# Kernel optimization log

Hardware: AMD Instinct MI355X
Metric: run time of the kernel (lower is better)

The kernel has to match this reference:

```python
import jax, jax.numpy as jnp
import numpy as np

N = 50000   # nodes
E = 800000  # edges (avg degree 16)
D = 128     # in_features == out_features (residual)
NEG_SLOPE = 0.2
BN_EPS = 1e-5


def setup_inputs() -> dict:
    key = jax.random.key(0)
    ks = jax.random.split(key, 8)
    x = jax.random.normal(ks[0], (N, D), jnp.float32)
    edge_index = jax.random.randint(ks[1], (2, E), 0, N, dtype=jnp.int32)
    W = jax.random.normal(ks[2], (D, D), jnp.float32) * 0.05
    att_src = jax.random.normal(ks[3], (D,), jnp.float32) * 0.1
    att_dst = jax.random.normal(ks[4], (D,), jnp.float32) * 0.1
    bias = jax.random.normal(ks[5], (D,), jnp.float32) * 0.01
    gamma = jnp.ones((D,), jnp.float32) + jax.random.normal(ks[6], (D,), jnp.float32) * 0.05
    beta = jax.random.normal(ks[7], (D,), jnp.float32) * 0.05
    return {"x": x, "edge_index": edge_index, "W": W, "att_src": att_src,
            "att_dst": att_dst, "bias": bias, "gamma": gamma, "beta": beta}


def reference(x, edge_index, W, att_src, att_dst, bias, gamma, beta):
    src, dst = edge_index[0], edge_index[1]
    # Linear transform (GATConv lin)
    h = x @ W                                   # [N, D]
    # Per-node attention logit halves
    a_s = h @ att_src                           # [N]
    a_d = h @ att_dst                           # [N]
    # Per-edge logits + LeakyReLU
    e = jax.nn.leaky_relu(a_s[src] + a_d[dst], NEG_SLOPE)  # [E]
    # Segment softmax over destination neighborhoods
    m = jax.ops.segment_max(e, dst, num_segments=N)        # [N]
    m = jnp.where(jnp.isfinite(m), m, 0.0)
    p = jnp.exp(e - m[dst])                                 # [E]
    denom = jax.ops.segment_sum(p, dst, num_segments=N)    # [N]
    alpha = p / denom[dst]                                  # [E]
    # Scatter-aggregate weighted neighbor features
    y = jax.ops.segment_sum(alpha[:, None] * h[src], dst, num_segments=N)  # [N, D]
    y = y + bias
    # NormDropRes (eval mode): BN with running_mean=0, running_var=1; dropout off
    yn = gamma * (y / jnp.sqrt(1.0 + BN_EPS)) + beta
    yn = jax.nn.relu(yn)
    # residual: in==out so base = x
    return x + yn
```

## Files before the change

kernel.cpp:

```cpp
#include <hip/hip_runtime.h>
#include <math.h>

#define NN 50000
#define EE 800000
#define DD 128
#define NEG 0.2f
#define SLOT 48
#define NWIN 512
#define WIN 98
#define CAP 2048

typedef short bf16x8 __attribute__((ext_vector_type(8)));
typedef float f32x4  __attribute__((ext_vector_type(4)));
typedef int   i32x4  __attribute__((ext_vector_type(4)));

__device__ __forceinline__ unsigned short f2bf(float f) {
    unsigned u = __float_as_uint(f);
    unsigned r = u + 0x7fffu + ((u >> 16) & 1u);
    return (unsigned short)(r >> 16);
}

__global__ __launch_bounds__(256) void k_pre(
        const float* __restrict__ W, unsigned short* __restrict__ wt,
        int* __restrict__ win_cnt)
{
    const int t = threadIdx.x;
    if (blockIdx.x == 64) {
        for (int i = t; i < NWIN; i += 256) win_cnt[i] = 0;
        return;
    }
    int idx = blockIdx.x * 256 + t;
    int k = idx >> 7, n = idx & 127;
    wt[n * DD + k] = f2bf(W[idx]);
}

#define XS_STRIDE 136
__global__ __launch_bounds__(256) void k_A(
        const float* __restrict__ x, const unsigned short* __restrict__ wtg,
        const float* __restrict__ att_src, const float* __restrict__ att_dst,
        unsigned short* __restrict__ hb, float* __restrict__ a_s, float* __restrict__ a_d,
        const int* __restrict__ ei, int* __restrict__ win_cnt, unsigned* __restrict__ pairs)
{
    __shared__ __align__(16) short smem[26112];
    const int t = threadIdx.x;

    if (blockIdx.x & 1) {
        int* lcnt  = (int*)smem;
        int* lbase = (int*)smem + NWIN;
        for (int i = t; i < NWIN; i += 256) lcnt[i] = 0;
        __syncthreads();

        int idx = (int)(blockIdx.x >> 1) * 256 + t;
        int b[4], lp[4];
        unsigned v[4];
        bool valid = idx < EE / 4;
        if (valid) {
            i32x4 s4 = __builtin_nontemporal_load(&((const i32x4*)ei)[idx]);
            i32x4 d4 = __builtin_nontemporal_load(&((const i32x4*)(ei + EE))[idx]);
            b[0] = d4.x / WIN; v[0] = ((unsigned)(d4.x - b[0] * WIN) << 16) | (unsigned)s4.x;
            b[1] = d4.y / WIN; v[1] = ((unsigned)(d4.y - b[1] * WIN) << 16) | (unsigned)s4.y;
            b[2] = d4.z / WIN; v[2] = ((unsigned)(d4.z - b[2] * WIN) << 16) | (unsigned)s4.z;
            b[3] = d4.w / WIN; v[3] = ((unsigned)(d4.w - b[3] * WIN) << 16) | (unsigned)s4.w;
            lp[0] = atomicAdd(&lcnt[b[0]], 1);
            lp[1] = atomicAdd(&lcnt[b[1]], 1);
            lp[2] = atomicAdd(&lcnt[b[2]], 1);
            lp[3] = atomicAdd(&lcnt[b[3]], 1);
        }
        __syncthreads();
        for (int i = t; i < NWIN; i += 256) {
            int c = lcnt[i];
            lbase[i] = c ? atomicAdd(&win_cnt[i], c) : 0;
        }
        __syncthreads();
        if (valid) {
#pragma unroll
            for (int k = 0; k < 4; k++) {
                int pos = lbase[b[k]] + lp[k];
                if (pos < CAP) pairs[(size_t)b[k] * CAP + pos] = v[k];
            }
        }
        return;
    }

    short* xs = smem;
    short* ws = smem + 64 * XS_STRIDE;
    const int row0 = (int)(blockIdx.x >> 1) * 64;

#pragma unroll
    for (int i = 0; i < 4; i++) {
        int idx = t + i * 256;
        int m = idx >> 4, c = idx & 15;
        int row = row0 + m;
        float4 f0 = make_float4(0.f, 0.f, 0.f, 0.f), f1 = f0;
        if (row < NN) {
            const float* p = x + (size_t)row * DD + c * 8;
            f0 = *(const float4*)p;
            f1 = *(const float4*)(p + 4);
        }
        bf16x8 v;
        v[0] = (short)f2bf(f0.x); v[1] = (short)f2bf(f0.y);
        v[2] = (short)f2bf(f0.z); v[3] = (short)f2bf(f0.w);
        v[4] = (short)f2bf(f1.x); v[5] = (short)f2bf(f1.y);
        v[6] = (short)f2bf(f1.z); v[7] = (short)f2bf(f1.w);
        *(bf16x8*)&xs[m * XS_STRIDE + c * 8] = v;
    }
#pragma unroll
    for (int i = 0; i < 8; i++) {
        int idx = t + i * 256;
        int n = idx >> 4, c = idx & 15;
        uint4 v = ((const uint4*)wtg)[idx];
        *(uint4*)&ws[n * XS_STRIDE + c * 8] = v;
    }
    __syncthreads();

    const int wv = t >> 6;
    const int lane = t & 63;
    const int n0 = lane & 15;
    const int quad = lane >> 4;

    bf16x8 afr[4];
#pragma unroll
    for (int kc = 0; kc < 4; kc++)
        afr[kc] = *(const bf16x8*)&xs[(wv * 16 + n0) * XS_STRIDE + kc * 32 + quad * 8];

    f32x4 acc[8];
#pragma unroll
    for (int nt = 0; nt < 8; nt++) {
        f32x4 a = {0.f, 0.f, 0.f, 0.f};
#pragma unroll
        for (int kc = 0; kc < 4; kc++) {
            bf16x8 bfr = *(const bf16x8*)&ws[(nt * 16 + n0) * XS_STRIDE + kc * 32 + quad * 8];
            a = __builtin_amdgcn_mfma_f32_16x16x32_bf16(afr[kc], bfr, a, 0, 0, 0);
        }
        acc[nt] = a;
    }

    const int rbase = row0 + wv * 16 + quad * 4;
    float ss[4] = {0.f, 0.f, 0.f, 0.f};
    float sd[4] = {0.f, 0.f, 0.f, 0.f};
#pragma unroll
    for (int nt = 0; nt < 8; nt++) {
        int col = nt * 16 + n0;
        float asc = att_src[col], adc = att_dst[col];
#pragma unroll
        for (int r = 0; r < 4; r++) {
            float v = acc[nt][r];
            ss[r] = fmaf(v, asc, ss[r]);
            sd[r] = fmaf(v, adc, sd[r]);
            int row = rbase + r;
            if (row < NN) hb[(size_t)row * DD + col] = f2bf(v);
        }
    }
#pragma unroll
    for (int r = 0; r < 4; r++) {
#pragma unroll
        for (int off = 1; off < 16; off <<= 1) {
            ss[r] += __shfl_xor(ss[r], off);
            sd[r] += __shfl_xor(sd[r], off);
        }
    }
    if (n0 == 0) {
#pragma unroll
        for (int r = 0; r < 4; r++) {
            int row = rbase + r;
            if (row < NN) { a_s[row] = ss[r]; a_d[row] = sd[r]; }
        }
    }
}

__global__ __launch_bounds__(1024) void k_BN(
        const int* __restrict__ win_cnt, const unsigned* __restrict__ pairs,
        const float* __restrict__ a_s, const float* __restrict__ a_d,
        const unsigned short* __restrict__ hb, const float* __restrict__ x,
        const float* __restrict__ bias, const float* __restrict__ gamma,
        const float* __restrict__ beta, float* __restrict__ out)
{
    __shared__ int lcur[WIN];
    __shared__ __align__(16) unsigned short lslots[WIN * SLOT];
    const int t = threadIdx.x;
    const int w = (int)blockIdx.x;
    int nloc = NN - w * WIN;
    if (nloc <= 0) return;
    if (nloc > WIN) nloc = WIN;

    for (int i = t; i < WIN; i += 1024) lcur[i] = 0;
    __syncthreads();

    int n = win_cnt[w]; if (n > CAP) n = CAP;
    const unsigned* pw = pairs + (size_t)w * CAP;
    for (int g = t; g < n; g += 1024) {
        unsigned v = pw[g];
        int ld = (int)(v >> 16);
        int pos = atomicAdd(&lcur[ld], 1);
        if (pos < SLOT) lslots[ld * SLOT + pos] = (unsigned short)(v & 0xffffu);
    }
    __syncthreads();

    const int wv = t >> 6;
    const int lane = t & 63;
    const int eq = lane >> 4;
    const int fl = lane & 15;
    const float invbn = 0.9999950000374997f;

    for (int nl = wv; nl < nloc; nl += 16) {
        int node = w * WIN + nl;

        int deg = lcur[nl];
        deg = deg > SLOT ? SLOT : deg;
        float ad = a_d[node];

        int s = 0;
        float p = 0.f;
        if (lane < deg) {
            s = (int)lslots[nl * SLOT + lane];
            float e = a_s[s] + ad;
            e = e > 0.f ? e : NEG * e;
            p = __expf(e);
        }
        float l = p;
#pragma unroll
        for (int off = 32; off > 0; off >>= 1)
            l += __shfl_xor(l, off);

        float acc[8];
#pragma unroll
        for (int k = 0; k < 8; k++) acc[k] = 0.f;

        for (int tt = 0; tt < deg; tt += 8) {
            int i0 = tt + eq, i1 = tt + 4 + eq;
            int   st0 = __shfl(s, i0);
            int   st1 = __shfl(s, i1);
            float pt0 = __shfl(p, i0);
            float pt1 = __shfl(p, i1);
            uint4 hv0 = *(const uint4*)(hb + ((size_t)st0 << 7) + fl * 8);
            uint4 hv1 = *(const uint4*)(hb + ((size_t)st1 << 7) + fl * 8);
            acc[0] = fmaf(pt0, __uint_as_float(hv0.x << 16),          acc[0]);
            acc[1] = fmaf(pt0, __uint_as_float(hv0.x & 0xffff0000u),  acc[1]);
            acc[2] = fmaf(pt0, __uint_as_float(hv0.y << 16),          acc[2]);
            acc[3] = fmaf(pt0, __uint_as_float(hv0.y & 0xffff0000u),  acc[3]);
            acc[4] = fmaf(pt0, __uint_as_float(hv0.z << 16),          acc[4]);
            acc[5] = fmaf(pt0, __uint_as_float(hv0.z & 0xffff0000u),  acc[5]);
            acc[6] = fmaf(pt0, __uint_as_float(hv0.w << 16),          acc[6]);
            acc[7] = fmaf(pt0, __uint_as_float(hv0.w & 0xffff0000u),  acc[7]);
            acc[0] = fmaf(pt1, __uint_as_float(hv1.x << 16),          acc[0]);
            acc[1] = fmaf(pt1, __uint_as_float(hv1.x & 0xffff0000u),  acc[1]);
            acc[2] = fmaf(pt1, __uint_as_float(hv1.y << 16),          acc[2]);
            acc[3] = fmaf(pt1, __uint_as_float(hv1.y & 0xffff0000u),  acc[3]);
            acc[4] = fmaf(pt1, __uint_as_float(hv1.z << 16),          acc[4]);
            acc[5] = fmaf(pt1, __uint_as_float(hv1.z & 0xffff0000u),  acc[5]);
            acc[6] = fmaf(pt1, __uint_as_float(hv1.w << 16),          acc[6]);
            acc[7] = fmaf(pt1, __uint_as_float(hv1.w & 0xffff0000u),  acc[7]);
        }

#pragma unroll
        for (int off = 16; off < 64; off <<= 1) {
#pragma unroll
            for (int k = 0; k < 8; k++)
                acc[k] += __shfl_xor(acc[k], off);
        }

        if (eq == 0) {
            float invl = (deg > 0) ? 1.f / l : 0.f;
            int c0 = fl * 8;
            const float* bp = bias  + c0;
            const float* gp = gamma + c0;
            const float* ep = beta  + c0;
            const float* xp = x + ((size_t)node << 7) + c0;
            float* op = out + ((size_t)node << 7) + c0;
            float4 o0, o1;
            float* oo[2] = {(float*)&o0, (float*)&o1};
#pragma unroll
            for (int k = 0; k < 8; k++) {
                float y  = acc[k] * invl + bp[k];
                float yn = gp[k] * (y * invbn) + ep[k];
                yn = yn > 0.f ? yn : 0.f;
                oo[k >> 2][k & 3] = xp[k] + yn;
            }
            *(float4*)op       = o0;
            *(float4*)(op + 4) = o1;
        }
    }
}

extern "C" void kernel_launch(void* const* d_in, const int* in_sizes, int n_in,
                              void* d_out, int out_size, void* d_ws, size_t ws_size,
                              hipStream_t stream)
{
    const float* x     = (const float*)d_in[0];
    const int*   ei    = (const int*)  d_in[1];
    const float* W     = (const float*)d_in[2];
    const float* att_s = (const float*)d_in[3];
    const float* att_d = (const float*)d_in[4];
    const float* bias  = (const float*)d_in[5];
    const float* gamma = (const float*)d_in[6];
    const float* beta  = (const float*)d_in[7];
    float* out = (float*)d_out;

    int*            win_cnt = (int*)d_ws;
    unsigned*       pairs   = (unsigned*)(win_cnt + NWIN);
    float*          a_sv    = (float*)(pairs + (size_t)NWIN * CAP);
    float*          a_dv    = a_sv + NN;
    unsigned short* wtg     = (unsigned short*)(a_dv + NN);
    unsigned short* hb      = wtg + DD * DD;

    k_pre <<<65, 256, 0, stream>>>(W, wtg, win_cnt);
    k_A   <<<2 * ((NN + 63) / 64), 256, 0, stream>>>(x, wtg, att_s, att_d, hb,
                                                     a_sv, a_dv, ei, win_cnt, pairs);
    k_BN  <<<NWIN, 1024, 0, stream>>>(win_cnt, pairs, a_sv, a_dv,
                                      hb, x, bias, gamma, beta, out);
}
```

Baseline: 155.2 us.

## Halve aggregation windows, process two nodes per wave, use nontemporal loads/stores

Doubles the number of destination windows (half as many nodes each, smaller pair capacity) and launches 512-thread blocks for the aggregation kernel. Each wave now handles two destination nodes at once, interleaving their gathers to expose more memory-level parallelism. Nontemporal loads and stores are added for the pair list, residual input and output. Smaller CAP per window raises overflow risk, since pairs beyond capacity are dropped silently, and the per-wave register count grows.

```diff
diff --git a/kernel.cpp b/kernel.cpp
--- a/kernel.cpp
+++ b/kernel.cpp
@@ -6,9 +6,9 @@
 #define DD 128
 #define NEG 0.2f
 #define SLOT 48
-#define NWIN 512
-#define WIN 98
-#define CAP 2048
+#define NWIN 1024
+#define WIN 49
+#define CAP 1024
 
 typedef short bf16x8 __attribute__((ext_vector_type(8)));
 typedef float f32x4  __attribute__((ext_vector_type(4)));
@@ -168,7 +168,7 @@
     }
 }
 
-__global__ __launch_bounds__(1024) void k_BN(
+__global__ __launch_bounds__(512) void k_BN(
         const int* __restrict__ win_cnt, const unsigned* __restrict__ pairs,
         const float* __restrict__ a_s, const float* __restrict__ a_d,
         const unsigned short* __restrict__ hb, const float* __restrict__ x,
@@ -183,13 +183,13 @@
     if (nloc <= 0) return;
     if (nloc > WIN) nloc = WIN;
 
-    for (int i = t; i < WIN; i += 1024) lcur[i] = 0;
+    if (t < WIN) lcur[t] = 0;
     __syncthreads();
 
     int n = win_cnt[w]; if (n > CAP) n = CAP;
     const unsigned* pw = pairs + (size_t)w * CAP;
-    for (int g = t; g < n; g += 1024) {
-        unsigned v = pw[g];
+    for (int g = t; g < n; g += 512) {
+        unsigned v = __builtin_nontemporal_load(&pw[g]);
         int ld = (int)(v >> 16);
         int pos = atomicAdd(&lcur[ld], 1);
         if (pos < SLOT) lslots[ld * SLOT + pos] = (unsigned short)(v & 0xffffu);
@@ -202,82 +202,155 @@
     const int fl = lane & 15;
     const float invbn = 0.9999950000374997f;
 
-    for (int nl = wv; nl < nloc; nl += 16) {
-        int node = w * WIN + nl;
-
-        int deg = lcur[nl];
-        deg = deg > SLOT ? SLOT : deg;
-        float ad = a_d[node];
-
-        int s = 0;
-        float p = 0.f;
-        if (lane < deg) {
-            s = (int)lslots[nl * SLOT + lane];
-            float e = a_s[s] + ad;
+    for (int base = 0; base < nloc; base += 16) {
+        int nlA = base + wv;
+        if (nlA >= nloc) break;
+        int nlB = nlA + 8;
+        bool vB = nlB < nloc;
+
+        int nodeA = w * WIN + nlA;
+        int degA = lcur[nlA]; degA = degA > SLOT ? SLOT : degA;
+        float adA = a_d[nodeA];
+        int sA = 0; float pA = 0.f;
+        if (lane < degA) sA = (int)lslots[nlA * SLOT + lane];
+
+        int nodeB = 0, degB = 0, sB = 0;
+        float pB = 0.f, adB = 0.f;
+        if (vB) {
+            nodeB = w * WIN + nlB;
+            degB = lcur[nlB]; degB = degB > SLOT ? SLOT : degB;
+            adB = a_d[nodeB];
+            if (lane < degB) sB = (int)lslots[nlB * SLOT + lane];
+        }
+        float asA = (lane < degA) ? a_s[sA] : 0.f;
+        float asB = (vB && lane < degB) ? a_s[sB] : 0.f;
+        if (lane < degA) {
+            float e = asA + adA;
             e = e > 0.f ? e : NEG * e;
-            p = __expf(e);
-        }
-        float l = p;
-#pragma unroll
-        for (int off = 32; off > 0; off >>= 1)
-            l += __shfl_xor(l, off);
-
-        float acc[8];
-#pragma unroll
-        for (int k = 0; k < 8; k++) acc[k] = 0.f;
-
-        for (int tt = 0; tt < deg; tt += 8) {
-            int i0 = tt + eq, i1 = tt + 4 + eq;
-            int   st0 = __shfl(s, i0);
-            int   st1 = __shfl(s, i1);
-            float pt0 = __shfl(p, i0);
-            float pt1 = __shfl(p, i1);
-            uint4 hv0 = *(const uint4*)(hb + ((size_t)st0 << 7) + fl * 8);
-            uint4 hv1 = *(const uint4*)(hb + ((size_t)st1 << 7) + fl * 8);
-            acc[0] = fmaf(pt0, __uint_as_float(hv0.x << 16),          acc[0]);
-            acc[1] = fmaf(pt0, __uint_as_float(hv0.x & 0xffff0000u),  acc[1]);
-            acc[2] = fmaf(pt0, __uint_as_float(hv0.y << 16),          acc[2]);
-            acc[3] = fmaf(pt0, __uint_as_float(hv0.y & 0xffff0000u),  acc[3]);
-            acc[4] = fmaf(pt0, __uint_as_float(hv0.z << 16),          acc[4]);
-            acc[5] = fmaf(pt0, __uint_as_float(hv0.z & 0xffff0000u),  acc[5]);
-            acc[6] = fmaf(pt0, __uint_as_float(hv0.w << 16),          acc[6]);
-            acc[7] = fmaf(pt0, __uint_as_float(hv0.w & 0xffff0000u),  acc[7]);
-            acc[0] = fmaf(pt1, __uint_as_float(hv1.x << 16),          acc[0]);
-            acc[1] = fmaf(pt1, __uint_as_float(hv1.x & 0xffff0000u),  acc[1]);
-            acc[2] = fmaf(pt1, __uint_as_float(hv1.y << 16),          acc[2]);
-            acc[3] = fmaf(pt1, __uint_as_float(hv1.y & 0xffff0000u),  acc[3]);
-            acc[4] = fmaf(pt1, __uint_as_float(hv1.z << 16),          acc[4]);
-            acc[5] = fmaf(pt1, __uint_as_float(hv1.z & 0xffff0000u),  acc[5]);
-            acc[6] = fmaf(pt1, __uint_as_float(hv1.w << 16),          acc[6]);
-            acc[7] = fmaf(pt1, __uint_as_float(hv1.w & 0xffff0000u),  acc[7]);
+            pA = __expf(e);
+        }
+        if (vB && lane < degB) {
+            float e = asB + adB;
+            e = e > 0.f ? e : NEG * e;
+            pB = __expf(e);
+        }
+        float lSA = pA, lSB = pB;
+#pragma unroll
+        for (int off = 32; off > 0; off >>= 1) {
+            lSA += __shfl_xor(lSA, off);
+            lSB += __shfl_xor(lSB, off);
+        }
+
+        float accA[8], accB[8];
+#pragma unroll
+        for (int k = 0; k < 8; k++) { accA[k] = 0.f; accB[k] = 0.f; }
+
+        int degM = degA > degB ? degA : degB;
+        for (int tt = 0; tt < degM; tt += 8) {
+            bool dA = tt < degA;
+            bool dB = tt < degB;
+            uint4 hA0, hA1, hB0, hB1;
+            float ptA0 = 0.f, ptA1 = 0.f, ptB0 = 0.f, ptB1 = 0.f;
+            if (dA) {
+                int stA0 = __shfl(sA, tt + eq);
+                int stA1 = __shfl(sA, tt + 4 + eq);
+                ptA0 = __shfl(pA, tt + eq);
+                ptA1 = __shfl(pA, tt + 4 + eq);
+                hA0 = *(const uint4*)(hb + ((size_t)stA0 << 7) + fl * 8);
+                hA1 = *(const uint4*)(hb + ((size_t)stA1 << 7) + fl * 8);
+            }
+            if (dB) {
+                int stB0 = __shfl(sB, tt + eq);
+                int stB1 = __shfl(sB, tt + 4 + eq);
+                ptB0 = __shfl(pB, tt + eq);
+                ptB1 = __shfl(pB, tt + 4 + eq);
+                hB0 = *(const uint4*)(hb + ((size_t)stB0 << 7) + fl * 8);
+                hB1 = *(const uint4*)(hb + ((size_t)stB1 << 7) + fl * 8);
+            }
+            if (dA) {
+                accA[0] = fmaf(ptA0, __uint_as_float(hA0.x << 16),          accA[0]);
+                accA[1] = fmaf(ptA0, __uint_as_float(hA0.x & 0xffff0000u),  accA[1]);
+                accA[2] = fmaf(ptA0, __uint_as_float(hA0.y << 16),          accA[2]);
+                accA[3] = fmaf(ptA0, __uint_as_float(hA0.y & 0xffff0000u),  accA[3]);
+                accA[4] = fmaf(ptA0, __uint_as_float(hA0.z << 16),          accA[4]);
+                accA[5] = fmaf(ptA0, __uint_as_float(hA0.z & 0xffff0000u),  accA[5]);
+                accA[6] = fmaf(ptA0, __uint_as_float(hA0.w << 16),          accA[6]);
+                accA[7] = fmaf(ptA0, __uint_as_float(hA0.w & 0xffff0000u),  accA[7]);
+                accA[0] = fmaf(ptA1, __uint_as_float(hA1.x << 16),          accA[0]);
+                accA[1] = fmaf(ptA1, __uint_as_float(hA1.x & 0xffff0000u),  accA[1]);
+                accA[2] = fmaf(ptA1, __uint_as_float(hA1.y << 16),          accA[2]);
+                accA[3] = fmaf(ptA1, __uint_as_float(hA1.y & 0xffff0000u),  accA[3]);
+                accA[4] = fmaf(ptA1, __uint_as_float(hA1.z << 16),          accA[4]);
+                accA[5] = fmaf(ptA1, __uint_as_float(hA1.z & 0xffff0000u),  accA[5]);
+                accA[6] = fmaf(ptA1, __uint_as_float(hA1.w << 16),          accA[6]);
+                accA[7] = fmaf(ptA1, __uint_as_float(hA1.w & 0xffff0000u),  accA[7]);
+            }
+            if (dB) {
+                accB[0] = fmaf(ptB0, __uint_as_float(hB0.x << 16),          accB[0]);
+                accB[1] = fmaf(ptB0, __uint_as_float(hB0.x & 0xffff0000u),  accB[1]);
+                accB[2] = fmaf(ptB0, __uint_as_float(hB0.y << 16),          accB[2]);
+                accB[3] = fmaf(ptB0, __uint_as_float(hB0.y & 0xffff0000u),  accB[3]);
+                accB[4] = fmaf(ptB0, __uint_as_float(hB0.z << 16),          accB[4]);
+                accB[5] = fmaf(ptB0, __uint_as_float(hB0.z & 0xffff0000u),  accB[5]);
+                accB[6] = fmaf(ptB0, __uint_as_float(hB0.w << 16),          accB[6]);
+                accB[7] = fmaf(ptB0, __uint_as_float(hB0.w & 0xffff0000u),  accB[7]);
+                accB[0] = fmaf(ptB1, __uint_as_float(hB1.x << 16),          accB[0]);
+                accB[1] = fmaf(ptB1, __uint_as_float(hB1.x & 0xffff0000u),  accB[1]);
+                accB[2] = fmaf(ptB1, __uint_as_float(hB1.y << 16),          accB[2]);
+                accB[3] = fmaf(ptB1, __uint_as_float(hB1.y & 0xffff0000u),  accB[3]);
+                accB[4] = fmaf(ptB1, __uint_as_float(hB1.z << 16),          accB[4]);
+                accB[5] = fmaf(ptB1, __uint_as_float(hB1.z & 0xffff0000u),  accB[5]);
+                accB[6] = fmaf(ptB1, __uint_as_float(hB1.w << 16),          accB[6]);
+                accB[7] = fmaf(ptB1, __uint_as_float(hB1.w & 0xffff0000u),  accB[7]);
+            }
         }
 
 #pragma unroll
         for (int off = 16; off < 64; off <<= 1) {
 #pragma unroll
-            for (int k = 0; k < 8; k++)
-                acc[k] += __shfl_xor(acc[k], off);
+            for (int k = 0; k < 8; k++) {
+                accA[k] += __shfl_xor(accA[k], off);
+                accB[k] += __shfl_xor(accB[k], off);
+            }
         }
 
         if (eq == 0) {
-            float invl = (deg > 0) ? 1.f / l : 0.f;
             int c0 = fl * 8;
             const float* bp = bias  + c0;
             const float* gp = gamma + c0;
             const float* ep = beta  + c0;
-            const float* xp = x + ((size_t)node << 7) + c0;
-            float* op = out + ((size_t)node << 7) + c0;
-            float4 o0, o1;
-            float* oo[2] = {(float*)&o0, (float*)&o1};
-#pragma unroll
-            for (int k = 0; k < 8; k++) {
-                float y  = acc[k] * invl + bp[k];
-                float yn = gp[k] * (y * invbn) + ep[k];
-                yn = yn > 0.f ? yn : 0.f;
-                oo[k >> 2][k & 3] = xp[k] + yn;
-            }
-            *(float4*)op       = o0;
-            *(float4*)(op + 4) = o1;
+            {
+                float invl = (degA > 0) ? 1.f / lSA : 0.f;
+                const float* xp = x + ((size_t)nodeA << 7) + c0;
+                float* op = out + ((size_t)nodeA << 7) + c0;
+                f32x4 o0, o1;
+#pragma unroll
+                for (int k = 0; k < 8; k++) {
+                    float y  = accA[k] * invl + bp[k];
+                    float yn = gp[k] * (y * invbn) + ep[k];
+                    yn = yn > 0.f ? yn : 0.f;
+                    float ov = __builtin_nontemporal_load(&xp[k]) + yn;
+                    if (k < 4) o0[k] = ov; else o1[k - 4] = ov;
+                }
+                __builtin_nontemporal_store(o0, (f32x4*)op);
+                __builtin_nontemporal_store(o1, (f32x4*)(op + 4));
+            }
+            if (vB) {
+                float invl = (degB > 0) ? 1.f / lSB : 0.f;
+                const float* xp = x + ((size_t)nodeB << 7) + c0;
+                float* op = out + ((size_t)nodeB << 7) + c0;
+                f32x4 o0, o1;
+#pragma unroll
+                for (int k = 0; k < 8; k++) {
+                    float y  = accB[k] * invl + bp[k];
+                    float yn = gp[k] * (y * invbn) + ep[k];
+                    yn = yn > 0.f ? yn : 0.f;
+                    float ov = __builtin_nontemporal_load(&xp[k]) + yn;
+                    if (k < 4) o0[k] = ov; else o1[k - 4] = ov;
+                }
+                __builtin_nontemporal_store(o0, (f32x4*)op);
+                __builtin_nontemporal_store(o1, (f32x4*)(op + 4));
+            }
         }
     }
 }
@@ -306,6 +379,6 @@
     k_pre <<<65, 256, 0, stream>>>(W, wtg, win_cnt);
     k_A   <<<2 * ((NN + 63) / 64), 256, 0, stream>>>(x, wtg, att_s, att_d, hb,
                                                      a_sv, a_dv, ei, win_cnt, pairs);
-    k_BN  <<<NWIN, 1024, 0, stream>>>(win_cnt, pairs, a_sv, a_dv,
-                                      hb, x, bias, gamma, beta, out);
-}
+    k_BN  <<<NWIN, 512, 0, stream>>>(win_cnt, pairs, a_sv, a_dv,
+                                     hb, x, bias, gamma, beta, out);
+}
```

After: 166.7 us. +7.4%, slower.

## Locally sort edges per block before scattering into destination windows

Applied to the files above, without the earlier changes.

Edge-binning blocks now each handle 4096 edges instead of 1024. Each block sorts its edges by destination window in shared memory using a prefix scan, then writes them out in runs so the global stores to the pairs buffer are contiguous. The grid interleaves one binning block per four GEMM blocks, which changes the GEMM row mapping and lowers the number of binning blocks and global atomics. The cost is extra shared-memory work, more registers per thread (16 edges each), and fewer binning blocks available to run in parallel.

```diff
diff --git a/kernel.cpp b/kernel.cpp
--- a/kernel.cpp
+++ b/kernel.cpp
@@ -9,6 +9,9 @@
 #define NWIN 512
 #define WIN 98
 #define CAP 2048
+#define EBLK 4096
+#define NEB 196
+#define GRID_A 980
 
 typedef short bf16x8 __attribute__((ext_vector_type(8)));
 typedef float f32x4  __attribute__((ext_vector_type(4)));
@@ -43,48 +46,85 @@
 {
     __shared__ __align__(16) short smem[26112];
     const int t = threadIdx.x;
-
-    if (blockIdx.x & 1) {
-        int* lcnt  = (int*)smem;
-        int* lbase = (int*)smem + NWIN;
+    const int bid = (int)blockIdx.x;
+
+    if (bid % 5 == 4) {
+        int*      lcnt   = (int*)smem;
+        int*      lpre   = (int*)smem + 512;
+        int*      gbase  = (int*)smem + 1024;
+        unsigned* sorted = (unsigned*)smem + 1536;
+        int*      wsum   = (int*)smem + 5632;
+
+        const int eb = bid / 5;
+        const int estart = eb * EBLK;
+        int ecnt = EE - estart; if (ecnt > EBLK) ecnt = EBLK;
+
         for (int i = t; i < NWIN; i += 256) lcnt[i] = 0;
         __syncthreads();
 
-        int idx = (int)(blockIdx.x >> 1) * 256 + t;
-        int b[4], lp[4];
-        unsigned v[4];
-        bool valid = idx < EE / 4;
-        if (valid) {
-            i32x4 s4 = __builtin_nontemporal_load(&((const i32x4*)ei)[idx]);
-            i32x4 d4 = __builtin_nontemporal_load(&((const i32x4*)(ei + EE))[idx]);
-            b[0] = d4.x / WIN; v[0] = ((unsigned)(d4.x - b[0] * WIN) << 16) | (unsigned)s4.x;
-            b[1] = d4.y / WIN; v[1] = ((unsigned)(d4.y - b[1] * WIN) << 16) | (unsigned)s4.y;
-            b[2] = d4.z / WIN; v[2] = ((unsigned)(d4.z - b[2] * WIN) << 16) | (unsigned)s4.z;
-            b[3] = d4.w / WIN; v[3] = ((unsigned)(d4.w - b[3] * WIN) << 16) | (unsigned)s4.w;
-            lp[0] = atomicAdd(&lcnt[b[0]], 1);
-            lp[1] = atomicAdd(&lcnt[b[1]], 1);
-            lp[2] = atomicAdd(&lcnt[b[2]], 1);
-            lp[3] = atomicAdd(&lcnt[b[3]], 1);
-        }
-        __syncthreads();
+        unsigned vv[16];
+        unsigned short off16[16];
+#pragma unroll
+        for (int j = 0; j < 16; j++) {
+            int li = j * 256 + t;
+            if (li < ecnt) {
+                int idx = estart + li;
+                int s = ei[idx];
+                int d = ei[EE + idx];
+                int b = d / WIN;
+                int ld = d - b * WIN;
+                vv[j] = ((unsigned)b << 23) | ((unsigned)ld << 16) | (unsigned)s;
+                off16[j] = (unsigned short)atomicAdd(&lcnt[b], 1);
+            }
+        }
+        __syncthreads();
+
+        int c0 = lcnt[2 * t], c1 = lcnt[2 * t + 1];
+        int sum = c0 + c1;
+        int lane = t & 63, wid = t >> 6;
+        int inc = sum;
+#pragma unroll
+        for (int off = 1; off < 64; off <<= 1) {
+            int u = __shfl_up(inc, off);
+            if (lane >= off) inc += u;
+        }
+        if (lane == 63) wsum[wid] = inc;
+        __syncthreads();
+        int wadd = 0;
+        for (int k = 0; k < wid; k++) wadd += wsum[k];
+        int ex = inc - sum + wadd;
+        lpre[2 * t] = ex;
+        lpre[2 * t + 1] = ex + c0;
         for (int i = t; i < NWIN; i += 256) {
             int c = lcnt[i];
-            lbase[i] = c ? atomicAdd(&win_cnt[i], c) : 0;
-        }
-        __syncthreads();
-        if (valid) {
-#pragma unroll
-            for (int k = 0; k < 4; k++) {
-                int pos = lbase[b[k]] + lp[k];
-                if (pos < CAP) pairs[(size_t)b[k] * CAP + pos] = v[k];
+            gbase[i] = c ? atomicAdd(&win_cnt[i], c) : 0;
+        }
+        __syncthreads();
+
+#pragma unroll
+        for (int j = 0; j < 16; j++) {
+            int li = j * 256 + t;
+            if (li < ecnt) {
+                unsigned v = vv[j];
+                int b = (int)(v >> 23);
+                sorted[lpre[b] + (int)off16[j]] = v;
             }
+        }
+        __syncthreads();
+
+        for (int i = t; i < ecnt; i += 256) {
+            unsigned w = sorted[i];
+            int b = (int)(w >> 23);
+            int pos = gbase[b] + (i - lpre[b]);
+            if (pos < CAP) pairs[(size_t)b * CAP + pos] = w & 0x7FFFFFu;
         }
         return;
     }
 
     short* xs = smem;
     short* ws = smem + 64 * XS_STRIDE;
-    const int row0 = (int)(blockIdx.x >> 1) * 64;
+    const int gord = (bid / 5) * 4 + (bid % 5);
+    const int row0 = gord * 64;
 
 #pragma unroll
     for (int i = 0; i < 4; i++) {
@@ -304,8 +344,8 @@
     unsigned short* hb      = wtg + DD * DD;
 
     k_pre <<<65, 256, 0, stream>>>(W, wtg, win_cnt);
-    k_A   <<<2 * ((NN + 63) / 64), 256, 0, stream>>>(x, wtg, att_s, att_d, hb,
-                                                     a_sv, a_dv, ei, win_cnt, pairs);
+    k_A   <<<GRID_A, 256, 0, stream>>>(x, wtg, att_s, att_d, hb,
+                                       a_sv, a_dv, ei, win_cnt, pairs);
     k_BN  <<<NWIN, 1024, 0, stream>>>(win_cnt, pairs, a_sv, a_dv,
                                       hb, x, bias, gamma, beta, out);
 }
```

Measured after the change: 146.3 us. 1.06x faster.
